# Optimization experiments

Hardware: AMD Instinct MI355X
Metric: run time of the kernel (lower is better)

Reference implementation:

```python
import jax, jax.numpy as jnp
import numpy as np

B, N, C = 8, 2048, 256
E = 32768
H, C_OUT = 8, 64
NEG_SLOPE = 0.2


def setup_inputs() -> dict:
    key = jax.random.key(0)
    k1, k2, k3, k4, k5 = jax.random.split(key, 5)
    x = jax.random.normal(k1, (B, N, C), dtype=jnp.float32)
    edge_index = jax.random.randint(k2, (2, E), 0, N, dtype=jnp.int64)
    W_lin = jax.random.normal(k3, (C, H * C_OUT), dtype=jnp.float32) * 0.05
    att_src = jax.random.normal(k4, (H, C_OUT), dtype=jnp.float32) * 0.05
    att_dst = jax.random.normal(k5, (H, C_OUT), dtype=jnp.float32) * 0.05
    bias = jnp.zeros((H * C_OUT,), dtype=jnp.float32)
    return {"x": x, "edge_index": edge_index, "W_lin": W_lin,
            "att_src": att_src, "att_dst": att_dst, "bias": bias}


def _segment_softmax(logits, segment_ids, num_segments):
    # stable softmax over edges grouped by destination node
    seg_max = jax.ops.segment_max(logits, segment_ids, num_segments=num_segments)
    logits = logits - seg_max[segment_ids]
    exp = jnp.exp(logits)
    seg_sum = jax.ops.segment_sum(exp, segment_ids, num_segments=num_segments)
    return exp / (seg_sum[segment_ids] + 1e-16)


def reference(x, edge_index, W_lin, att_src, att_dst, bias):
    Bn = B * N
    # node linear projection -> [B*N, H, C_out]
    xt = (x.reshape(Bn, C) @ W_lin).reshape(Bn, H, C_OUT)

    # batch the shared edge_index: block b offset by b*N, then append self-loops
    offs = (jnp.arange(B, dtype=edge_index.dtype) * N)[None, :, None]  # [1,B,1]
    ei = (edge_index[:, None, :] + offs).reshape(2, B * E)              # [2,B*E]
    loops = jnp.arange(Bn, dtype=edge_index.dtype)
    src = jnp.concatenate([ei[0], loops])
    dst = jnp.concatenate([ei[1], loops])

    x_j = xt[src]  # [E_tot, H, C_out] source features
    x_i = xt[dst]
    alpha = jnp.einsum('ehc,hc->eh', x_j, att_src) + jnp.einsum('ehc,hc->eh', x_i, att_dst)
    alpha = jax.nn.leaky_relu(alpha, NEG_SLOPE)
    alpha = _segment_softmax(alpha, dst, Bn)  # softmax over incoming edges per node/head

    msg = x_j * alpha[:, :, None]
    out = jax.ops.segment_sum(msg, dst, num_segments=Bn)  # [B*N, H, C_out]
    out = out.reshape(B, N, H * C_OUT) + bias
    return out
```

## Files before the change

kernel.cpp:

```cpp
#include <hip/hip_runtime.h>
#include <hip/hip_bf16.h>

#define BDIM 8
#define NNODE 2048
#define CIN 256
#define NEDGE 32768
#define NHEAD 8
#define COUT 64
#define HC 512
#define BN_TOT 16384
#define NEG_SLOPE 0.2f
#define GEMM_BLKS 256
#define CAP 64

typedef __hip_bfloat16 bf16;
typedef __attribute__((ext_vector_type(8))) short bfrag;
typedef __attribute__((ext_vector_type(4))) float ffrag;
typedef float f32x2 __attribute__((ext_vector_type(2)));
typedef float fv4 __attribute__((ext_vector_type(4)));

static __device__ __forceinline__ short f2b(float f) {
    __hip_bfloat16 h = __float2bfloat16(f);
    return *(short*)&h;
}
static __device__ __forceinline__ unsigned pack2(float a, float b) {
    return (unsigned)(unsigned short)f2b(a) | ((unsigned)(unsigned short)f2b(b) << 16);
}
static __device__ __forceinline__ void pkfma(f32x2& a, f32x2 x, f32x2 w) {
    asm("v_pk_fma_f32 %0, %1, %2, %0" : "+v"(a) : "v"(x), "v"(w));
}
static __device__ __forceinline__ f32x2 unpack2(unsigned v) {
    f32x2 r;
    r.x = __uint_as_float(v << 16);
    r.y = __uint_as_float(v & 0xffff0000u);
    return r;
}
static __device__ __forceinline__ void async_cp16(const short* gsrc, short* ldst) {
    __builtin_amdgcn_global_load_lds(
        (const __attribute__((address_space(1))) void*)gsrc,
        (__attribute__((address_space(3))) void*)ldst, 16, 0, 0);
}

__global__ __launch_bounds__(256) void prep_kernel(const float* __restrict__ W,
                                                   short* __restrict__ WT,
                                                   int* __restrict__ cnt) {
    const int b = blockIdx.x;
    if (b < 128) {
        __shared__ float t[32][33];
        const int kt = b >> 4;
        const int nt = b & 15;
        const int tx = threadIdx.x & 31, ty = threadIdx.x >> 5;
#pragma unroll
        for (int i = 0; i < 4; ++i)
            t[ty + 8 * i][tx] = W[(kt * 32 + ty + 8 * i) * HC + nt * 32 + tx];
        __syncthreads();
#pragma unroll
        for (int i = 0; i < 4; ++i)
            WT[(nt * 32 + ty + 8 * i) * CIN + kt * 32 + tx] = f2b(t[tx][ty + 8 * i]);
    } else {
        for (int k = threadIdx.x; k < NNODE; k += 256) cnt[k] = 0;
    }
}

__global__ __launch_bounds__(512, 2) void gemm_scatter(const float* __restrict__ x,
                                                       const short* __restrict__ WT,
                                                       short* __restrict__ xtb,
                                                       const float* __restrict__ att_src,
                                                       const float* __restrict__ att_dst,
                                                       float* __restrict__ ssrc,
                                                       float* __restrict__ sdst,
                                                       const int* __restrict__ ei,
                                                       int* __restrict__ cnt,
                                                       int* __restrict__ col) {
    __shared__ __align__(16) short As[64 * 256];
    __shared__ __align__(16) short Bs[2][512 * 32];

    const int gblk = blockIdx.x;
    const int tid  = threadIdx.x;

    if (gblk < 64) {
        const int t = gblk * 512 + tid;
        const int s = ei[t];
        const int d = ei[NEDGE + t];
        const int p = atomicAdd(&cnt[d], 1);
        if (p < CAP) col[d * CAP + p] = s;
    }

    const int tile = (gblk & 7) * 32 + (gblk >> 3);
    const int lane = tid & 63;
    const int w    = tid >> 6;
    const int row0 = tile * 64;
    const int fm   = lane & 15;
    const int fq   = lane >> 4;

    {
        const int r   = tid >> 3;
        const int kb0 = (tid & 7) * 8;
#pragma unroll
        for (int i = 0; i < 4; ++i) {
            const int kb = kb0 + i * 64;
            fv4 v0 = __builtin_nontemporal_load((const fv4*)&x[(row0 + r) * CIN + kb]);
            fv4 v1 = __builtin_nontemporal_load((const fv4*)&x[(row0 + r) * CIN + kb + 4]);
            bfrag o;
            o[0] = f2b(v0.x); o[1] = f2b(v0.y); o[2] = f2b(v0.z); o[3] = f2b(v0.w);
            o[4] = f2b(v1.x); o[5] = f2b(v1.y); o[6] = f2b(v1.z); o[7] = f2b(v1.w);
            *(bfrag*)&As[(((r >> 4) * 32 + (kb >> 3)) * 16 + (r & 15)) * 8] = o;
        }
    }

    {
#pragma unroll
        for (int i2 = 0; i2 < 4; ++i2) {
            const int cb16 = w * 4 + i2;
            const int c = cb16 * 16 + (lane >> 2);
            async_cp16(&WT[c * CIN + (lane & 3) * 8], &Bs[0][cb16 * 512]);
        }
    }
    __syncthreads();

    ffrag acc[4][4] = {};

#pragma unroll
    for (int k8 = 0; k8 < 8; ++k8) {
        const int buf = k8 & 1;
        if (k8 < 7) {
            asm volatile("s_waitcnt lgkmcnt(0)" ::: "memory");
            __builtin_amdgcn_sched_barrier(0);
            const int k0n = (k8 + 1) * 32;
#pragma unroll
            for (int i2 = 0; i2 < 4; ++i2) {
                const int cb16 = w * 4 + i2;
                const int c = cb16 * 16 + (lane >> 2);
                async_cp16(&WT[c * CIN + k0n + (lane & 3) * 8], &Bs[buf ^ 1][cb16 * 512]);
            }
            asm volatile("s_waitcnt vmcnt(4)" ::: "memory");
        } else {
            asm volatile("s_waitcnt vmcnt(0)" ::: "memory");
        }
        __builtin_amdgcn_sched_barrier(0);

        bfrag af[4], bfv[4];
#pragma unroll
        for (int mg = 0; mg < 4; ++mg)
            af[mg] = *(const bfrag*)&As[((mg * 32 + k8 * 4 + fq) * 16 + fm) * 8];
#pragma unroll
        for (int ng = 0; ng < 4; ++ng)
            bfv[ng] = *(const bfrag*)&Bs[buf][(((w * 4 + ng) * 16 + fm) * 4 + fq) * 8];
#pragma unroll
        for (int ng = 0; ng < 4; ++ng)
#pragma unroll
            for (int mg = 0; mg < 4; ++mg)
                acc[mg][ng] = __builtin_amdgcn_mfma_f32_16x16x32_bf16(
                    bfv[ng], af[mg], acc[mg][ng], 0, 0, 0);
    }

    float4 s4[4], d4[4];
#pragma unroll
    for (int ng = 0; ng < 4; ++ng) {
        const int cb = w * 64 + ng * 16 + fq * 4;
        s4[ng] = *(const float4*)&att_src[cb];
        d4[ng] = *(const float4*)&att_dst[cb];
    }
#pragma unroll
    for (int mg = 0; mg < 4; ++mg) {
        const int nd = row0 + mg * 16 + fm;
        float ps = 0.f, pd = 0.f;
#pragma unroll
        for (int ng = 0; ng < 4; ++ng) {
            const int cb = w * 64 + ng * 16 + fq * 4;
            uint2 pk;
            pk.x = pack2(acc[mg][ng][0], acc[mg][ng][1]);
            pk.y = pack2(acc[mg][ng][2], acc[mg][ng][3]);
            *(uint2*)&xtb[nd * HC + cb] = pk;
            ps += acc[mg][ng][0] * s4[ng].x + acc[mg][ng][1] * s4[ng].y +
                  acc[mg][ng][2] * s4[ng].z + acc[mg][ng][3] * s4[ng].w;
            pd += acc[mg][ng][0] * d4[ng].x + acc[mg][ng][1] * d4[ng].y +
                  acc[mg][ng][2] * d4[ng].z + acc[mg][ng][3] * d4[ng].w;
        }
        ps += __shfl_xor(ps, 16); ps += __shfl_xor(ps, 32);
        pd += __shfl_xor(pd, 16); pd += __shfl_xor(pd, 32);
        if (lane < 16) {
            ssrc[nd * NHEAD + w] = ps;
            sdst[nd * NHEAD + w] = pd;
        }
    }
}

__global__ __launch_bounds__(256) void aggregate(const short* __restrict__ xtb,
                                                 const float* __restrict__ ssrc,
                                                 const float* __restrict__ sdst,
                                                 const int* __restrict__ cnt,
                                                 const int* __restrict__ col,
                                                 const float* __restrict__ bias,
                                                 float* __restrict__ out) {
    const int lane = threadIdx.x & 63;
    const int nb   = threadIdx.x >> 6;
    const int blk  = blockIdx.x;
    const int bidx = blk & 7;
    const int boff = bidx * NNODE;
    const int i    = boff + (blk >> 3) * 4 + nb;
    const int n    = i & (NNODE - 1);
    const int deg  = min(cnt[n], CAP);
    const int start = n * CAP;
    const int h    = lane >> 3;
    const int sub  = lane & 7;
    const int c8   = lane * 8;

    const float sdh = sdst[i * NHEAD + h];
    float selfv = ssrc[i * NHEAD + h] + sdh;
    selfv = selfv >= 0.f ? selfv : NEG_SLOPE * selfv;
    const float eself = __expf(selfv);

    f32x2 acc2[4] = {};

    {
        uint4 xv = *(const uint4*)&xtb[i * HC + c8];
        f32x2 ev = {eself, eself};
        pkfma(acc2[0], unpack2(xv.x), ev);
        pkfma(acc2[1], unpack2(xv.y), ev);
        pkfma(acc2[2], unpack2(xv.z), ev);
        pkfma(acc2[3], unpack2(xv.w), ev);
    }

    float sp = 0.f;
    for (int e0 = 0; e0 < deg; e0 += 8) {
        int jme = i;
        float wv = 0.f;
        if (e0 + sub < deg) {
            jme = boff + col[start + e0 + sub];
            float v = ssrc[jme * NHEAD + h] + sdh;
            v = v >= 0.f ? v : NEG_SLOPE * v;
            wv = __expf(v);
        }
        sp += wv;
#pragma unroll
        for (int k = 0; k < 8; ++k) {
            const int   jk = __shfl(jme, k);
            const float wk = __shfl(wv, (h << 3) | k);
            uint4 xr = *(const uint4*)&xtb[jk * HC + c8];
            f32x2 wk2 = {wk, wk};
            pkfma(acc2[0], unpack2(xr.x), wk2);
            pkfma(acc2[1], unpack2(xr.y), wk2);
            pkfma(acc2[2], unpack2(xr.z), wk2);
            pkfma(acc2[3], unpack2(xr.w), wk2);
        }
    }
    sp += __shfl_xor(sp, 4); sp += __shfl_xor(sp, 2); sp += __shfl_xor(sp, 1);
    const float inv = 1.f / (sp + eself + 1e-16f);

    const float4 b0 = *(const float4*)&bias[c8];
    const float4 b1 = *(const float4*)&bias[c8 + 4];
    fv4 o0 = {acc2[0].x * inv + b0.x, acc2[0].y * inv + b0.y,
              acc2[1].x * inv + b0.z, acc2[1].y * inv + b0.w};
    fv4 o1 = {acc2[2].x * inv + b1.x, acc2[2].y * inv + b1.y,
              acc2[3].x * inv + b1.z, acc2[3].y * inv + b1.w};
    __builtin_nontemporal_store(o0, (fv4*)&out[i * HC + c8]);
    __builtin_nontemporal_store(o1, (fv4*)&out[i * HC + c8 + 4]);
}

extern "C" void kernel_launch(void* const* d_in, const int* in_sizes, int n_in,
                              void* d_out, int out_size, void* d_ws, size_t ws_size,
                              hipStream_t stream) {
    const float* x       = (const float*)d_in[0];
    const int*   ei      = (const int*)d_in[1];
    const float* W       = (const float*)d_in[2];
    const float* att_src = (const float*)d_in[3];
    const float* att_dst = (const float*)d_in[4];
    const float* bias    = (const float*)d_in[5];
    float* out = (float*)d_out;

    char* ws = (char*)d_ws;
    short* xtb  = (short*)(ws);
    float* ssrc = (float*)(ws + 16777216);
    float* sdst = (float*)(ws + 17301504);
    int*   cnt  = (int*)(ws + 17825792);
    int*   col  = (int*)(ws + 17833984);
    short* WT   = (short*)(ws + 18358272);
    prep_kernel<<<129, 256, 0, stream>>>(W, WT, cnt);
    gemm_scatter<<<GEMM_BLKS, 512, 0, stream>>>(x, WT, xtb, att_src, att_dst,
                                                ssrc, sdst, ei, cnt, col);
    aggregate<<<BN_TOT / 4, 256, 0, stream>>>(xtb, ssrc, sdst, cnt, col, bias, out);
}
```

Measured before the change: 120.2 us.

## Triple-buffer W tiles and stream x loads across the GEMM k-loop

Moves from double to triple buffering of the weight tiles in LDS, issuing async copies two k-steps ahead. The x tile is no longer converted to bf16 all at once up front. Its k-slices are loaded into registers and written to LDS incrementally between MFMA steps, so global loads overlap compute. This adds more LDS (a third B buffer), a per-iteration barrier, and hand-tuned vmcnt counts that must match the issue order exactly. Any mismatch risks races.

```diff
diff --git a/kernel.cpp b/kernel.cpp
--- a/kernel.cpp
+++ b/kernel.cpp
@@ -15,6 +15,7 @@
 
 typedef __hip_bfloat16 bf16;
 typedef __attribute__((ext_vector_type(8))) short bfrag;
+typedef __attribute__((ext_vector_type(4))) short bhalf;
 typedef __attribute__((ext_vector_type(4))) float ffrag;
 typedef float f32x2 __attribute__((ext_vector_type(2)));
 typedef float fv4 __attribute__((ext_vector_type(4)));
@@ -73,7 +74,7 @@
                                                        int* __restrict__ cnt,
                                                        int* __restrict__ col) {
     __shared__ __align__(16) short As[64 * 256];
-    __shared__ __align__(16) short Bs[2][512 * 32];
+    __shared__ __align__(16) short Bs[3][512 * 32];
 
     const int gblk = blockIdx.x;
     const int tid  = threadIdx.x;
@@ -84,6 +85,8 @@
         const int d = ei[NEDGE + t];
         const int p = atomicAdd(&cnt[d], 1);
         if (p < CAP) col[d * CAP + p] = s;
+        asm volatile("s_waitcnt vmcnt(0)" ::: "memory");
+        __builtin_amdgcn_sched_barrier(0);
     }
 
     const int tile = (gblk & 7) * 32 + (gblk >> 3);
@@ -93,66 +96,111 @@
     const int fm   = lane & 15;
     const int fq   = lane >> 4;
 
+    const int arow = tid >> 3;
+    const int akq  = (tid & 7) * 4;
+    const float* xrow = &x[(row0 + arow) * CIN];
+    short* awp = &As[(((arow >> 4) * 32) * 16 + (arow & 15)) * 8];
+#define A_WRITE(r, v)                                                          \
+    {                                                                          \
+        const int k_ = (r) * 32 + akq;                                         \
+        bhalf o_;                                                              \
+        o_[0] = f2b((v).x); o_[1] = f2b((v).y);                                \
+        o_[2] = f2b((v).z); o_[3] = f2b((v).w);                                \
+        *(bhalf*)&awp[((k_ >> 3) * 16) * 8 + (k_ & 7)] = o_;                   \
+    }
+
     {
-        const int r   = tid >> 3;
-        const int kb0 = (tid & 7) * 8;
-#pragma unroll
-        for (int i = 0; i < 4; ++i) {
-            const int kb = kb0 + i * 64;
-            fv4 v0 = __builtin_nontemporal_load((const fv4*)&x[(row0 + r) * CIN + kb]);
-            fv4 v1 = __builtin_nontemporal_load((const fv4*)&x[(row0 + r) * CIN + kb + 4]);
-            bfrag o;
-            o[0] = f2b(v0.x); o[1] = f2b(v0.y); o[2] = f2b(v0.z); o[3] = f2b(v0.w);
-            o[4] = f2b(v1.x); o[5] = f2b(v1.y); o[6] = f2b(v1.z); o[7] = f2b(v1.w);
-            *(bfrag*)&As[(((r >> 4) * 32 + (kb >> 3)) * 16 + (r & 15)) * 8] = o;
-        }
-    }
-
-    {
+        fv4 a0 = __builtin_nontemporal_load((const fv4*)&xrow[akq]);
+        fv4 a1 = __builtin_nontemporal_load((const fv4*)&xrow[32 + akq]);
+        A_WRITE(0, a0);
+        A_WRITE(1, a1);
+    }
+    __builtin_amdgcn_sched_barrier(0);
+#pragma unroll
+    for (int c2 = 0; c2 < 2; ++c2) {
 #pragma unroll
         for (int i2 = 0; i2 < 4; ++i2) {
             const int cb16 = w * 4 + i2;
             const int c = cb16 * 16 + (lane >> 2);
-            async_cp16(&WT[c * CIN + (lane & 3) * 8], &Bs[0][cb16 * 512]);
-        }
-    }
-    __syncthreads();
+            async_cp16(&WT[c * CIN + c2 * 32 + (lane & 3) * 8], &Bs[c2][cb16 * 512]);
+        }
+    }
+    __builtin_amdgcn_sched_barrier(0);
+    fv4 xreg[8];
+#pragma unroll
+    for (int r = 2; r < 6; ++r)
+        xreg[r] = __builtin_nontemporal_load((const fv4*)&xrow[r * 32 + akq]);
+    __builtin_amdgcn_sched_barrier(0);
+
+    asm volatile("s_waitcnt lgkmcnt(0)" ::: "memory");
+    __builtin_amdgcn_sched_barrier(0);
+    __builtin_amdgcn_s_barrier();
 
     ffrag acc[4][4] = {};
+    const int BCNT[8] = {13, 14, 10, 9, 8, 8, 4, 0};
 
 #pragma unroll
     for (int k8 = 0; k8 < 8; ++k8) {
-        const int buf = k8 & 1;
-        if (k8 < 7) {
+        if (k8 < 6) {
             asm volatile("s_waitcnt lgkmcnt(0)" ::: "memory");
             __builtin_amdgcn_sched_barrier(0);
-            const int k0n = (k8 + 1) * 32;
+            const int bb = (k8 + 2) % 3;
+            const int k0n = (k8 + 2) * 32;
 #pragma unroll
             for (int i2 = 0; i2 < 4; ++i2) {
                 const int cb16 = w * 4 + i2;
                 const int c = cb16 * 16 + (lane >> 2);
-                async_cp16(&WT[c * CIN + k0n + (lane & 3) * 8], &Bs[buf ^ 1][cb16 * 512]);
+                async_cp16(&WT[c * CIN + k0n + (lane & 3) * 8], &Bs[bb][cb16 * 512]);
             }
-            asm volatile("s_waitcnt vmcnt(4)" ::: "memory");
-        } else {
-            asm volatile("s_waitcnt vmcnt(0)" ::: "memory");
+            __builtin_amdgcn_sched_barrier(0);
+        }
+        if (k8 < 2) {
+            xreg[k8 + 6] = __builtin_nontemporal_load(
+                (const fv4*)&xrow[(k8 + 6) * 32 + akq]);
+            __builtin_amdgcn_sched_barrier(0);
+        }
+        switch (k8) {
+            case 0: asm volatile("s_waitcnt vmcnt(13)" ::: "memory"); break;
+            case 1: asm volatile("s_waitcnt vmcnt(14)" ::: "memory"); break;
+            case 2: asm volatile("s_waitcnt vmcnt(10)" ::: "memory"); break;
+            case 3: asm volatile("s_waitcnt vmcnt(9)"  ::: "memory"); break;
+            case 4: asm volatile("s_waitcnt vmcnt(8)"  ::: "memory"); break;
+            case 5: asm volatile("s_waitcnt vmcnt(8)"  ::: "memory"); break;
+            case 6: asm volatile("s_waitcnt vmcnt(4)"  ::: "memory"); break;
+            default: asm volatile("s_waitcnt vmcnt(0)" ::: "memory"); break;
         }
         __builtin_amdgcn_sched_barrier(0);
 
+        const int br = k8 % 3;
         bfrag af[4], bfv[4];
 #pragma unroll
         for (int mg = 0; mg < 4; ++mg)
             af[mg] = *(const bfrag*)&As[((mg * 32 + k8 * 4 + fq) * 16 + fm) * 8];
 #pragma unroll
         for (int ng = 0; ng < 4; ++ng)
-            bfv[ng] = *(const bfrag*)&Bs[buf][(((w * 4 + ng) * 16 + fm) * 4 + fq) * 8];
+            bfv[ng] = *(const bfrag*)&Bs[br][(((w * 4 + ng) * 16 + fm) * 4 + fq) * 8];
 #pragma unroll
         for (int ng = 0; ng < 4; ++ng)
 #pragma unroll
             for (int mg = 0; mg < 4; ++mg)
                 acc[mg][ng] = __builtin_amdgcn_mfma_f32_16x16x32_bf16(
                     bfv[ng], af[mg], acc[mg][ng], 0, 0, 0);
-    }
+
+        if (k8 < 6) {
+            switch (k8) {
+                case 0: A_WRITE(2, xreg[2]); break;
+                case 1: A_WRITE(3, xreg[3]); break;
+                case 2: A_WRITE(4, xreg[4]); break;
+                case 3: A_WRITE(5, xreg[5]); break;
+                case 4: A_WRITE(6, xreg[6]); break;
+                default: A_WRITE(7, xreg[7]); break;
+            }
+        }
+        asm volatile("s_waitcnt lgkmcnt(0)" ::: "memory");
+        __builtin_amdgcn_sched_barrier(0);
+        __builtin_amdgcn_s_barrier();
+    }
+#undef A_WRITE
 
     float4 s4[4], d4[4];
 #pragma unroll
```

New measurement: 123.3 us. 2.6% more time.
